# Kernel tuning notes

Hardware: AMD Instinct MI355X
Metric: run time of the kernel (lower is better)

The kernel has to match this reference:

```python
import jax, jax.numpy as jnp
import numpy as np

N_POL, N_TICK, N_COMM = 50000, 200000, 5000
N_STATES, N_SECTORS, N_INDUSTRIES = 50, 12, 150
EMB, HID, OUT = 32, 64, 32
N_NODES = N_POL + N_TICK + N_COMM
N_EDGES = 4_000_000


def setup_inputs() -> dict:
    key = jax.random.key(0)
    ks = jax.random.split(key, 24)
    s = lambda d: 1.0 / np.sqrt(d)
    inp = {
        "pol_features": jax.random.normal(ks[0], (N_POL, 7), jnp.float32),
        "state_ids": jax.random.randint(ks[1], (N_POL,), 0, N_STATES, jnp.int32),
        "sector_ids": jax.random.randint(ks[2], (N_TICK,), 0, N_SECTORS, jnp.int32),
        "industry_ids": jax.random.randint(ks[3], (N_TICK,), 0, N_INDUSTRIES, jnp.int32),
        "comp_extra": jax.random.normal(ks[4], (N_TICK, 1), jnp.float32),
        "edge_index": jax.random.randint(ks[5], (2, N_EDGES), 0, N_NODES, jnp.int32),
        "edge_weight": jax.random.uniform(ks[6], (N_EDGES,), jnp.float32),
        # learned params
        "pol_W": jax.random.normal(ks[7], (7, EMB), jnp.float32) * s(7),
        "pol_b": jnp.zeros((EMB,), jnp.float32),
        "state_emb": jax.random.normal(ks[8], (N_STATES, EMB), jnp.float32),
        "sector_emb": jax.random.normal(ks[9], (N_SECTORS, 8), jnp.float32),
        "industry_emb": jax.random.normal(ks[10], (N_INDUSTRIES, 8), jnp.float32),
        "comp_W": jax.random.normal(ks[11], (17, EMB), jnp.float32) * s(17),
        "comp_b": jnp.zeros((EMB,), jnp.float32),
        "comm_emb": jax.random.normal(ks[12], (N_COMM, EMB), jnp.float32),
        "ln_g": jnp.ones((EMB,), jnp.float32),
        "ln_b": jnp.zeros((EMB,), jnp.float32),
        "w1_rel": jax.random.normal(ks[13], (EMB, HID), jnp.float32) * s(EMB),
        "b1_rel": jnp.zeros((HID,), jnp.float32),
        "w1_root": jax.random.normal(ks[14], (EMB, HID), jnp.float32) * s(EMB),
        "w2_rel": jax.random.normal(ks[15], (HID, OUT), jnp.float32) * s(HID),
        "b2_rel": jnp.zeros((OUT,), jnp.float32),
        "w2_root": jax.random.normal(ks[16], (HID, OUT), jnp.float32) * s(HID),
    }
    return inp


def _layernorm(x, g, b, eps=1e-5):
    mu = jnp.mean(x, axis=-1, keepdims=True)
    var = jnp.mean(jnp.square(x - mu), axis=-1, keepdims=True)
    return (x - mu) * jax.lax.rsqrt(var + eps) * g + b


def _graph_conv(x, src, dst, ew, w_rel, b_rel, w_root):
    # PyG GraphConv: out = lin_rel(sum_{j->i} w_ji * x_j) + lin_root(x_i)
    msg = x[src] * ew[:, None]                                   # [E, d] gather
    agg = jax.ops.segment_sum(msg, dst, num_segments=x.shape[0])  # [N, d] scatter
    return agg @ w_rel + b_rel + x @ w_root


def reference(pol_features, state_ids, sector_ids, industry_ids, comp_extra,
              edge_index, edge_weight,
              pol_W, pol_b, state_emb, sector_emb, industry_emb, comp_W, comp_b,
              comm_emb, ln_g, ln_b, w1_rel, b1_rel, w1_root, w2_rel, b2_rel, w2_root):
    pol = jax.nn.relu(pol_features @ pol_W + pol_b) + state_emb[state_ids]
    comp_in = jnp.concatenate(
        [sector_emb[sector_ids], industry_emb[industry_ids], comp_extra], axis=1)  # [n_tick,17]
    comp = jax.nn.relu(comp_in @ comp_W + comp_b)
    x = jnp.concatenate([pol, comp, comm_emb], axis=0)  # [N, EMB]
    x = _layernorm(x, ln_g, ln_b)
    src, dst = edge_index[0], edge_index[1]
    x = jax.nn.relu(_graph_conv(x, src, dst, edge_weight, w1_rel, b1_rel, w1_root))
    # dropout omitted (eval mode)
    x = _graph_conv(x, src, dst, edge_weight, w2_rel, b2_rel, w2_root)
    return x
```

## Files before the change

kernel.cpp:

```cpp
#include <hip/hip_runtime.h>
#include <hip/hip_bf16.h>

#define N_POL  50000
#define N_TICK 200000
#define N_COMM 5000
#define N_NODES 255000
#define N_EDGES 4000000
#define EMB 32
#define HID 64
#define OUT_D 32

__global__ __launch_bounds__(256) void k_embed(
    const float* __restrict__ pol_features, const int* __restrict__ state_ids,
    const int* __restrict__ sector_ids, const int* __restrict__ industry_ids,
    const float* __restrict__ comp_extra,
    const float* __restrict__ pol_W, const float* __restrict__ pol_b,
    const float* __restrict__ state_emb, const float* __restrict__ sector_emb,
    const float* __restrict__ industry_emb, const float* __restrict__ comp_W,
    const float* __restrict__ comp_b, const float* __restrict__ comm_emb,
    const float* __restrict__ ln_g, const float* __restrict__ ln_b,
    float* __restrict__ x)
{
    int tid = blockIdx.x * 256 + threadIdx.x;
    int r = tid >> 5;
    int c = tid & 31;
    if (r >= N_NODES) return;

    float acc;
    if (r < N_POL) {
        acc = pol_b[c];
        #pragma unroll
        for (int k = 0; k < 7; ++k)
            acc = fmaf(pol_features[r*7 + k], pol_W[k*EMB + c], acc);
        acc = fmaxf(acc, 0.f);
        acc += state_emb[state_ids[r]*EMB + c];
    } else if (r < N_POL + N_TICK) {
        int i = r - N_POL;
        acc = comp_b[c];
        int sec = sector_ids[i], ind = industry_ids[i];
        #pragma unroll
        for (int k = 0; k < 8; ++k)
            acc = fmaf(sector_emb[sec*8 + k], comp_W[k*EMB + c], acc);
        #pragma unroll
        for (int k = 0; k < 8; ++k)
            acc = fmaf(industry_emb[ind*8 + k], comp_W[(8+k)*EMB + c], acc);
        acc = fmaf(comp_extra[i], comp_W[16*EMB + c], acc);
        acc = fmaxf(acc, 0.f);
    } else {
        acc = comm_emb[(r - N_POL - N_TICK)*EMB + c];
    }

    float s = acc;
    #pragma unroll
    for (int m = 16; m >= 1; m >>= 1) s += __shfl_xor(s, m, 32);
    float mu = s * (1.f/32.f);
    float d  = acc - mu;
    float v  = d * d;
    #pragma unroll
    for (int m = 16; m >= 1; m >>= 1) v += __shfl_xor(v, m, 32);
    v *= (1.f/32.f);
    x[r*EMB + c] = d * rsqrtf(v + 1e-5f) * ln_g[c] + ln_b[c];
}

__global__ __launch_bounds__(256) void k_hist(const int* __restrict__ ei,
                                              int* __restrict__ deg)
{
    int e = blockIdx.x * 256 + threadIdx.x;
    if (e >= N_EDGES) return;
    atomicAdd(&deg[ei[N_EDGES + e]], 1);
}

__global__ __launch_bounds__(256) void k_scan1(const int* __restrict__ deg,
                                               int* __restrict__ rowptr,
                                               int* __restrict__ bsum)
{
    __shared__ int s[256];
    int t = threadIdx.x;
    int base = blockIdx.x * 1024 + t * 4;
    int d0 = (base+0 < N_NODES) ? deg[base+0] : 0;
    int d1 = (base+1 < N_NODES) ? deg[base+1] : 0;
    int d2 = (base+2 < N_NODES) ? deg[base+2] : 0;
    int d3 = (base+3 < N_NODES) ? deg[base+3] : 0;
    int tsum = d0 + d1 + d2 + d3;
    s[t] = tsum;
    __syncthreads();
    for (int off = 1; off < 256; off <<= 1) {
        int v = (t >= off) ? s[t-off] : 0;
        __syncthreads();
        s[t] += v;
        __syncthreads();
    }
    int excl = s[t] - tsum;
    if (base+0 < N_NODES) rowptr[base+0] = excl;
    if (base+1 < N_NODES) rowptr[base+1] = excl + d0;
    if (base+2 < N_NODES) rowptr[base+2] = excl + d0 + d1;
    if (base+3 < N_NODES) rowptr[base+3] = excl + d0 + d1 + d2;
    if (t == 255) bsum[blockIdx.x] = s[255];
}

#define NBLK_SCAN 250

__global__ __launch_bounds__(256) void k_scan2(int* bsum)
{
    __shared__ int s[256];
    int t = threadIdx.x;
    int v = (t < NBLK_SCAN) ? bsum[t] : 0;
    s[t] = v;
    __syncthreads();
    for (int off = 1; off < 256; off <<= 1) {
        int u = (t >= off) ? s[t-off] : 0;
        __syncthreads();
        s[t] += u;
        __syncthreads();
    }
    if (t < NBLK_SCAN) bsum[t] = s[t] - v;
}

__global__ __launch_bounds__(256) void k_scan3(int* __restrict__ rowptr,
                                               const int* __restrict__ bsum)
{
    int i = blockIdx.x * 256 + threadIdx.x;
    if (i < N_NODES) rowptr[i] += bsum[i >> 10];
    if (i == 0) rowptr[N_NODES] = N_EDGES;
}

__global__ __launch_bounds__(256) void k_fill(const int* __restrict__ ei,
                                              const float* __restrict__ ew,
                                              const int* __restrict__ rowptr,
                                              int* __restrict__ cur,
                                              int2* __restrict__ ce)
{
    int e = blockIdx.x * 256 + threadIdx.x;
    if (e >= N_EDGES) return;
    int dst = ei[N_EDGES + e];
    int pos = rowptr[dst] + atomicAdd(&cur[dst], 1);
    ce[pos] = make_int2(ei[e], __float_as_int(ew[e]));
}

__global__ __launch_bounds__(256) void k_agg(const int* __restrict__ rowptr,
                                             const int2* __restrict__ ce,
                                             const float* __restrict__ feat,
                                             float* __restrict__ agg)
{
    int tid = blockIdx.x * 256 + threadIdx.x;
    int r = tid >> 5;
    int c = tid & 31;
    if (r >= N_NODES) return;
    int beg = rowptr[r], end = rowptr[r+1];
    float a0 = 0.f, a1 = 0.f, a2 = 0.f, a3 = 0.f;
    int i = beg;
    for (; i + 4 <= end; i += 4) {
        int2 e0 = ce[i], e1 = ce[i+1], e2 = ce[i+2], e3 = ce[i+3];
        a0 = fmaf(feat[(size_t)e0.x*EMB + c], __int_as_float(e0.y), a0);
        a1 = fmaf(feat[(size_t)e1.x*EMB + c], __int_as_float(e1.y), a1);
        a2 = fmaf(feat[(size_t)e2.x*EMB + c], __int_as_float(e2.y), a2);
        a3 = fmaf(feat[(size_t)e3.x*EMB + c], __int_as_float(e3.y), a3);
    }
    for (; i < end; ++i) {
        int2 e = ce[i];
        a0 = fmaf(feat[(size_t)e.x*EMB + c], __int_as_float(e.y), a0);
    }
    agg[(size_t)r*EMB + c] = (a0 + a1) + (a2 + a3);
}

__global__ __launch_bounds__(256) void k_conv1(
    const float* __restrict__ x, const float* __restrict__ agg,
    const float* __restrict__ w1_rel, const float* __restrict__ b1_rel,
    const float* __restrict__ w1_root,
    float* __restrict__ x1)
{
    int lane = threadIdx.x & 63;
    int wid  = threadIdx.x >> 6;

    float wr[32], wt[32];
    #pragma unroll
    for (int k = 0; k < 32; ++k) {
        wr[k] = w1_rel[k*HID + lane];
        wt[k] = w1_root[k*HID + lane];
    }
    float bias = b1_rel[lane];

    int nw = gridDim.x * 4;
    for (int r0 = blockIdx.x*4 + wid; r0 < N_NODES; r0 += nw) {
        int r = __builtin_amdgcn_readfirstlane(r0);
        const float4* xr = (const float4*)(x   + (size_t)r*EMB);
        const float4* ar = (const float4*)(agg + (size_t)r*EMB);
        float a0 = bias, a1 = 0.f, a2 = 0.f, a3 = 0.f;
        #pragma unroll
        for (int i = 0; i < 8; ++i) {
            float4 xv = xr[i];
            float4 av = ar[i];
            a0 = fmaf(xv.x, wt[4*i+0], a0);  a0 = fmaf(av.x, wr[4*i+0], a0);
            a1 = fmaf(xv.y, wt[4*i+1], a1);  a1 = fmaf(av.y, wr[4*i+1], a1);
            a2 = fmaf(xv.z, wt[4*i+2], a2);  a2 = fmaf(av.z, wr[4*i+2], a2);
            a3 = fmaf(xv.w, wt[4*i+3], a3);  a3 = fmaf(av.w, wr[4*i+3], a3);
        }
        x1[(size_t)r*HID + lane] = fmaxf((a0 + a1) + (a2 + a3), 0.f);
    }
}

__global__ __launch_bounds__(256) void k_z(
    const float* __restrict__ x1, const float* __restrict__ w2_rel,
    float* __restrict__ z)
{
    int lane = threadIdx.x & 63;
    int wid  = threadIdx.x >> 6;
    int c    = lane & 31;
    int half = lane >> 5;

    float w[32];
    #pragma unroll
    for (int j = 0; j < 32; ++j) w[j] = w2_rel[(half*32 + j)*OUT_D + c];

    int nw = gridDim.x * 4;
    for (int r0 = blockIdx.x*4 + wid; r0 < N_NODES; r0 += nw) {
        int r = __builtin_amdgcn_readfirstlane(r0);
        const float4* xr = (const float4*)(x1 + (size_t)r*HID + half*32);
        float p0 = 0.f, p1 = 0.f, p2 = 0.f, p3 = 0.f;
        #pragma unroll
        for (int i = 0; i < 8; ++i) {
            float4 v = xr[i];
            p0 = fmaf(v.x, w[4*i+0], p0);
            p1 = fmaf(v.y, w[4*i+1], p1);
            p2 = fmaf(v.z, w[4*i+2], p2);
            p3 = fmaf(v.w, w[4*i+3], p3);
        }
        float part = (p0 + p1) + (p2 + p3);
        part += __shfl_xor(part, 32, 64);
        if (lane < 32) z[(size_t)r*EMB + c] = part;
    }
}

__global__ __launch_bounds__(256) void k_out(
    const float* __restrict__ x1, const float* __restrict__ agg,
    const float* __restrict__ w2_root, const float* __restrict__ b2_rel,
    float* __restrict__ out)
{
    int lane = threadIdx.x & 63;
    int wid  = threadIdx.x >> 6;
    int c    = lane & 31;
    int half = lane >> 5;

    float w[32];
    #pragma unroll
    for (int j = 0; j < 32; ++j) w[j] = w2_root[(half*32 + j)*OUT_D + c];
    float bias = b2_rel[c];

    int nw = gridDim.x * 4;
    for (int r0 = blockIdx.x*4 + wid; r0 < N_NODES; r0 += nw) {
        int r = __builtin_amdgcn_readfirstlane(r0);
        const float4* xr = (const float4*)(x1 + (size_t)r*HID + half*32);
        float p0 = 0.f, p1 = 0.f, p2 = 0.f, p3 = 0.f;
        #pragma unroll
        for (int i = 0; i < 8; ++i) {
            float4 v = xr[i];
            p0 = fmaf(v.x, w[4*i+0], p0);
            p1 = fmaf(v.y, w[4*i+1], p1);
            p2 = fmaf(v.z, w[4*i+2], p2);
            p3 = fmaf(v.w, w[4*i+3], p3);
        }
        float part = (p0 + p1) + (p2 + p3);
        part += __shfl_xor(part, 32, 64);
        if (lane < 32)
            out[(size_t)r*OUT_D + c] = part + agg[(size_t)r*EMB + c] + bias;
    }
}

extern "C" void kernel_launch(void* const* d_in, const int* in_sizes, int n_in,
                              void* d_out, int out_size, void* d_ws, size_t ws_size,
                              hipStream_t stream) {
    const float* pol_features = (const float*)d_in[0];
    const int*   state_ids    = (const int*)  d_in[1];
    const int*   sector_ids   = (const int*)  d_in[2];
    const int*   industry_ids = (const int*)  d_in[3];
    const float* comp_extra   = (const float*)d_in[4];
    const int*   edge_index   = (const int*)  d_in[5];
    const float* edge_weight  = (const float*)d_in[6];
    const float* pol_W        = (const float*)d_in[7];
    const float* pol_b        = (const float*)d_in[8];
    const float* state_emb    = (const float*)d_in[9];
    const float* sector_emb   = (const float*)d_in[10];
    const float* industry_emb = (const float*)d_in[11];
    const float* comp_W       = (const float*)d_in[12];
    const float* comp_b       = (const float*)d_in[13];
    const float* comm_emb     = (const float*)d_in[14];
    const float* ln_g         = (const float*)d_in[15];
    const float* ln_b         = (const float*)d_in[16];
    const float* w1_rel       = (const float*)d_in[17];
    const float* b1_rel       = (const float*)d_in[18];
    const float* w1_root      = (const float*)d_in[19];
    const float* w2_rel       = (const float*)d_in[20];
    const float* b2_rel       = (const float*)d_in[21];
    const float* w2_root      = (const float*)d_in[22];

    float* x   = (float*)d_ws;
    float* x1  = x  + (size_t)N_NODES * EMB;
    float* agg = x1 + (size_t)N_NODES * HID;
    int2*  ce  = (int2*)(agg + (size_t)N_NODES * EMB);
    int*   rowptr = (int*)(ce + N_EDGES);
    int*   cur    = rowptr + N_NODES + 8;
    int*   bsum   = cur + N_NODES + 8;
    float* out = (float*)d_out;

    k_embed<<<(N_NODES*32 + 255)/256, 256, 0, stream>>>(
        pol_features, state_ids, sector_ids, industry_ids, comp_extra,
        pol_W, pol_b, state_emb, sector_emb, industry_emb, comp_W, comp_b,
        comm_emb, ln_g, ln_b, x);

    hipMemsetAsync(cur, 0, (size_t)N_NODES * sizeof(int), stream);
    k_hist<<<(N_EDGES + 255)/256, 256, 0, stream>>>(edge_index, cur);
    k_scan1<<<NBLK_SCAN, 256, 0, stream>>>(cur, rowptr, bsum);
    k_scan2<<<1, 256, 0, stream>>>(bsum);
    k_scan3<<<(N_NODES + 255)/256, 256, 0, stream>>>(rowptr, bsum);
    hipMemsetAsync(cur, 0, (size_t)N_NODES * sizeof(int), stream);
    k_fill<<<(N_EDGES + 255)/256, 256, 0, stream>>>(edge_index, edge_weight,
                                                    rowptr, cur, ce);

    k_agg<<<(N_NODES*32 + 255)/256, 256, 0, stream>>>(rowptr, ce, x, agg);
    k_conv1<<<4096, 256, 0, stream>>>(x, agg, w1_rel, b1_rel, w1_root, x1);
    k_z<<<4096, 256, 0, stream>>>(x1, w2_rel,  x);

    k_agg<<<(N_NODES*32 + 255)/256, 256, 0, stream>>>(rowptr, ce,  x, agg);
    k_out<<<4096, 256, 0, stream>>>(x1, agg, w2_root, b2_rel, out);
}
```

Measured before the change: 921.7 us.

## Replace per-node CSR build with two-pass bucketed radix sort and LDS-atomic aggregation

Drops the per-node histogram, three-kernel scan and atomic fill that built a CSR. In their place, a two-level radix partition sorts edges by destination into 128-node groups: coarse 1024-node buckets first, then 8 sub-buckets each, with staging in LDS so global writes stay coalesced. Aggregation then runs one workgroup per group and accumulates into shared memory with workgroup-scope float atomics. This cuts global atomics and scattered writes, but adds LDS atomic contention, a non-deterministic summation order and packed src/row encodings that depend on the node count bounds.

```diff
diff --git a/kernel.cpp b/kernel.cpp
--- a/kernel.cpp
+++ b/kernel.cpp
@@ -9,6 +9,12 @@
 #define EMB 32
 #define HID 64
 #define OUT_D 32
+
+#define NG 1993
+#define NB 250
+#define CHUNK 4096
+#define NWG_A 977
+#define PARTS 5
 
 __global__ __launch_bounds__(256) void k_embed(
     const float* __restrict__ pol_features, const int* __restrict__ state_ids,
@@ -62,50 +68,38 @@
     x[r*EMB + c] = d * rsqrtf(v + 1e-5f) * ln_g[c] + ln_b[c];
 }
 
-__global__ __launch_bounds__(256) void k_hist(const int* __restrict__ ei,
-                                              int* __restrict__ deg)
-{
-    int e = blockIdx.x * 256 + threadIdx.x;
-    if (e >= N_EDGES) return;
-    atomicAdd(&deg[ei[N_EDGES + e]], 1);
-}
-
-__global__ __launch_bounds__(256) void k_scan1(const int* __restrict__ deg,
-                                               int* __restrict__ rowptr,
-                                               int* __restrict__ bsum)
+__global__ __launch_bounds__(256) void k_bhist(const int* __restrict__ ei,
+                                               int* __restrict__ gcnt)
+{
+    __shared__ int h[NG];
+    for (int j = threadIdx.x; j < NG; j += 256) h[j] = 0;
+    __syncthreads();
+    int e0 = blockIdx.x * CHUNK;
+    int n  = min(CHUNK, N_EDGES - e0);
+    for (int j = threadIdx.x; j < n; j += 256) {
+        int d = ei[N_EDGES + e0 + j];
+        atomicAdd(&h[d >> 7], 1);
+    }
+    __syncthreads();
+    for (int j = threadIdx.x; j < NG; j += 256)
+        if (h[j]) atomicAdd(&gcnt[j], h[j]);
+}
+
+__global__ __launch_bounds__(256) void k_bscan(int* __restrict__ cnt_then_cur,
+                                               int* __restrict__ groupBase,
+                                               int* __restrict__ curA)
 {
     __shared__ int s[256];
     int t = threadIdx.x;
-    int base = blockIdx.x * 1024 + t * 4;
-    int d0 = (base+0 < N_NODES) ? deg[base+0] : 0;
-    int d1 = (base+1 < N_NODES) ? deg[base+1] : 0;
-    int d2 = (base+2 < N_NODES) ? deg[base+2] : 0;
-    int d3 = (base+3 < N_NODES) ? deg[base+3] : 0;
-    int tsum = d0 + d1 + d2 + d3;
+    int v[8];
+    int tsum = 0;
+    #pragma unroll
+    for (int k = 0; k < 8; ++k) {
+        int j = t*8 + k;
+        v[k] = (j < NG) ? cnt_then_cur[j] : 0;
+        tsum += v[k];
+    }
     s[t] = tsum;
-    __syncthreads();
-    for (int off = 1; off < 256; off <<= 1) {
-        int v = (t >= off) ? s[t-off] : 0;
-        __syncthreads();
-        s[t] += v;
-        __syncthreads();
-    }
-    int excl = s[t] - tsum;
-    if (base+0 < N_NODES) rowptr[base+0] = excl;
-    if (base+1 < N_NODES) rowptr[base+1] = excl + d0;
-    if (base+2 < N_NODES) rowptr[base+2] = excl + d0 + d1;
-    if (base+3 < N_NODES) rowptr[base+3] = excl + d0 + d1 + d2;
-    if (t == 255) bsum[blockIdx.x] = s[255];
-}
-
-#define NBLK_SCAN 250
-
-__global__ __launch_bounds__(256) void k_scan2(int* bsum)
-{
-    __shared__ int s[256];
-    int t = threadIdx.x;
-    int v = (t < NBLK_SCAN) ? bsum[t] : 0;
-    s[t] = v;
     __syncthreads();
     for (int off = 1; off < 256; off <<= 1) {
         int u = (t >= off) ? s[t-off] : 0;
@@ -113,54 +107,156 @@
         s[t] += u;
         __syncthreads();
     }
-    if (t < NBLK_SCAN) bsum[t] = s[t] - v;
-}
-
-__global__ __launch_bounds__(256) void k_scan3(int* __restrict__ rowptr,
-                                               const int* __restrict__ bsum)
-{
-    int i = blockIdx.x * 256 + threadIdx.x;
-    if (i < N_NODES) rowptr[i] += bsum[i >> 10];
-    if (i == 0) rowptr[N_NODES] = N_EDGES;
-}
-
-__global__ __launch_bounds__(256) void k_fill(const int* __restrict__ ei,
-                                              const float* __restrict__ ew,
-                                              const int* __restrict__ rowptr,
-                                              int* __restrict__ cur,
-                                              int2* __restrict__ ce)
-{
-    int e = blockIdx.x * 256 + threadIdx.x;
-    if (e >= N_EDGES) return;
-    int dst = ei[N_EDGES + e];
-    int pos = rowptr[dst] + atomicAdd(&cur[dst], 1);
-    ce[pos] = make_int2(ei[e], __float_as_int(ew[e]));
-}
-
-__global__ __launch_bounds__(256) void k_agg(const int* __restrict__ rowptr,
-                                             const int2* __restrict__ ce,
-                                             const float* __restrict__ feat,
-                                             float* __restrict__ agg)
-{
-    int tid = blockIdx.x * 256 + threadIdx.x;
-    int r = tid >> 5;
-    int c = tid & 31;
-    if (r >= N_NODES) return;
-    int beg = rowptr[r], end = rowptr[r+1];
-    float a0 = 0.f, a1 = 0.f, a2 = 0.f, a3 = 0.f;
-    int i = beg;
-    for (; i + 4 <= end; i += 4) {
-        int2 e0 = ce[i], e1 = ce[i+1], e2 = ce[i+2], e3 = ce[i+3];
-        a0 = fmaf(feat[(size_t)e0.x*EMB + c], __int_as_float(e0.y), a0);
-        a1 = fmaf(feat[(size_t)e1.x*EMB + c], __int_as_float(e1.y), a1);
-        a2 = fmaf(feat[(size_t)e2.x*EMB + c], __int_as_float(e2.y), a2);
-        a3 = fmaf(feat[(size_t)e3.x*EMB + c], __int_as_float(e3.y), a3);
-    }
-    for (; i < end; ++i) {
-        int2 e = ce[i];
-        a0 = fmaf(feat[(size_t)e.x*EMB + c], __int_as_float(e.y), a0);
-    }
-    agg[(size_t)r*EMB + c] = (a0 + a1) + (a2 + a3);
+    int excl = s[t] - tsum;
+    int running = excl;
+    #pragma unroll
+    for (int k = 0; k < 8; ++k) {
+        int j = t*8 + k;
+        if (j < NG) {
+            groupBase[j] = running;
+            cnt_then_cur[j] = running;
+        }
+        running += v[k];
+    }
+    if (t < NB) curA[t] = excl;
+    if (t == 250) groupBase[NG] = excl;
+}
+
+__global__ __launch_bounds__(256) void k_passA(const int* __restrict__ ei,
+                                               const float* __restrict__ ew,
+                                               int* __restrict__ curA,
+                                               int2* __restrict__ ce1)
+{
+    __shared__ int2 stg[CHUNK];
+    __shared__ unsigned char aux[CHUNK];
+    __shared__ int cnt[256], start[256], mycur[256], goff[256], sc[256];
+
+    int t = threadIdx.x;
+    int e0 = blockIdx.x * CHUNK;
+    int n  = min(CHUNK, N_EDGES - e0);
+
+    cnt[t] = 0;
+    __syncthreads();
+    for (int j = t; j < n; j += 256) {
+        int d = ei[N_EDGES + e0 + j];
+        atomicAdd(&cnt[d >> 10], 1);
+    }
+    __syncthreads();
+    int v = cnt[t];
+    sc[t] = v;
+    __syncthreads();
+    for (int off = 1; off < 256; off <<= 1) {
+        int u = (t >= off) ? sc[t-off] : 0;
+        __syncthreads();
+        sc[t] += u;
+        __syncthreads();
+    }
+    start[t] = sc[t] - v;
+    mycur[t] = sc[t] - v;
+    if (t < NB && v > 0) goff[t] = atomicAdd(&curA[t], v);
+    __syncthreads();
+
+    for (int j = t; j < n; j += 256) {
+        int d = ei[N_EDGES + e0 + j];
+        int srcv = ei[e0 + j];
+        float w = ew[e0 + j];
+        int b = d >> 10;
+        int slot = atomicAdd(&mycur[b], 1);
+        stg[slot] = make_int2(((d & 1023) << 18) | srcv, __float_as_int(w));
+        aux[slot] = (unsigned char)b;
+    }
+    __syncthreads();
+    for (int j = t; j < n; j += 256) {
+        int b = aux[j];
+        ce1[goff[b] + (j - start[b])] = stg[j];
+    }
+}
+
+__global__ __launch_bounds__(256) void k_passA2(const int2* __restrict__ ce1,
+                                                const int* __restrict__ groupBase,
+                                                int* __restrict__ curA2,
+                                                int2* __restrict__ ce2)
+{
+    __shared__ int2 stg[CHUNK];
+    __shared__ unsigned char aux[CHUNK];
+    __shared__ int cnt[8], start[8], mycur[8], goff[8];
+
+    int t = threadIdx.x;
+    int b = blockIdx.x / PARTS;
+    int k = blockIdx.x % PARTS;
+    int g0 = b * 8;
+    int g1 = min(g0 + 8, NG);
+    int lo = groupBase[g0];
+    int hi = groupBase[g1];
+    int len = hi - lo;
+    int chunk = (len + PARTS - 1) / PARTS;
+    int s0 = lo + k * chunk;
+    int s1 = min(s0 + chunk, hi);
+    int n = s1 - s0;
+    if (n <= 0) return;
+
+    if (t < 8) cnt[t] = 0;
+    __syncthreads();
+    for (int j = t; j < n; j += 256) {
+        int p = ce1[s0 + j].x;
+        atomicAdd(&cnt[(p >> 25) & 7], 1);
+    }
+    __syncthreads();
+    if (t == 0) {
+        int running = 0;
+        #pragma unroll
+        for (int s = 0; s < 8; ++s) { start[s] = running; mycur[s] = running; running += cnt[s]; }
+    }
+    __syncthreads();
+    if (t < 8 && cnt[t] > 0) goff[t] = atomicAdd(&curA2[g0 + t], cnt[t]);
+    __syncthreads();
+
+    for (int j = t; j < n; j += 256) {
+        int2 e = ce1[s0 + j];
+        int sub = (e.x >> 25) & 7;
+        int slot = atomicAdd(&mycur[sub], 1);
+        stg[slot] = e;
+        aux[slot] = (unsigned char)sub;
+    }
+    __syncthreads();
+    for (int j = t; j < n; j += 256) {
+        int sub = aux[j];
+        ce2[goff[sub] + (j - start[sub])] = stg[j];
+    }
+}
+
+__global__ __launch_bounds__(256) void k_bagg(const int* __restrict__ groupBase,
+                                              const int2* __restrict__ ce2,
+                                              const float* __restrict__ feat,
+                                              float* __restrict__ agg)
+{
+    __shared__ float acc[128 * EMB];
+    int t = threadIdx.x;
+    int g = blockIdx.x;
+
+    float4* a4 = (float4*)acc;
+    #pragma unroll
+    for (int k = 0; k < 4; ++k) a4[t + k*256] = make_float4(0.f, 0.f, 0.f, 0.f);
+    __syncthreads();
+
+    int lo = groupBase[g], hi = groupBase[g + 1];
+    int grp = t >> 5;
+    int c   = t & 31;
+    for (int i = lo + grp; i < hi; i += 8) {
+        int2 e = ce2[i];
+        int row  = (e.x >> 18) & 127;
+        int srcv = e.x & 0x3FFFF;
+        float w  = __int_as_float(e.y);
+        float val = feat[(size_t)srcv * EMB + c] * w;
+        __hip_atomic_fetch_add(&acc[row * EMB + c], val,
+                               __ATOMIC_RELAXED, __HIP_MEMORY_SCOPE_WORKGROUP);
+    }
+    __syncthreads();
+
+    int r0 = g * 128;
+    int nr = min(128, N_NODES - r0);
+    for (int j = t; j < nr * EMB; j += 256)
+        agg[(size_t)r0 * EMB + j] = acc[j];
 }
 
 __global__ __launch_bounds__(256) void k_conv1(
@@ -296,30 +392,29 @@
     float* x   = (float*)d_ws;
     float* x1  = x  + (size_t)N_NODES * EMB;
     float* agg = x1 + (size_t)N_NODES * HID;
-    int2*  ce  = (int2*)(agg + (size_t)N_NODES * EMB);
-    int*   rowptr = (int*)(ce + N_EDGES);
-    int*   cur    = rowptr + N_NODES + 8;
-    int*   bsum   = cur + N_NODES + 8;
+    int2*  ce2 = (int2*)(agg + (size_t)N_NODES * EMB);
+    int*   groupBase = (int*)(ce2 + N_EDGES);
+    int*   curA2     = groupBase + NG + 8;
+    int*   curA      = curA2 + NG + 8;
+    int2*  ce1 = (int2*)x1;
     float* out = (float*)d_out;
+
+    hipMemsetAsync(curA2, 0, NG * sizeof(int), stream);
 
     k_embed<<<(N_NODES*32 + 255)/256, 256, 0, stream>>>(
         pol_features, state_ids, sector_ids, industry_ids, comp_extra,
         pol_W, pol_b, state_emb, sector_emb, industry_emb, comp_W, comp_b,
         comm_emb, ln_g, ln_b, x);
 
-    hipMemsetAsync(cur, 0, (size_t)N_NODES * sizeof(int), stream);
-    k_hist<<<(N_EDGES + 255)/256, 256, 0, stream>>>(edge_index, cur);
-    k_scan1<<<NBLK_SCAN, 256, 0, stream>>>(cur, rowptr, bsum);
-    k_scan2<<<1, 256, 0, stream>>>(bsum);
-    k_scan3<<<(N_NODES + 255)/256, 256, 0, stream>>>(rowptr, bsum);
-    hipMemsetAsync(cur, 0, (size_t)N_NODES * sizeof(int), stream);
-    k_fill<<<(N_EDGES + 255)/256, 256, 0, stream>>>(edge_index, edge_weight,
-                                                    rowptr, cur, ce);
-
-    k_agg<<<(N_NODES*32 + 255)/256, 256, 0, stream>>>(rowptr, ce, x, agg);
+    k_bhist<<<NWG_A, 256, 0, stream>>>(edge_index, curA2);
+    k_bscan<<<1, 256, 0, stream>>>(curA2, groupBase, curA);
+    k_passA<<<NWG_A, 256, 0, stream>>>(edge_index, edge_weight, curA, ce1);
+    k_passA2<<<NB*PARTS, 256, 0, stream>>>(ce1, groupBase, curA2, ce2);
+
+    k_bagg<<<NG, 256, 0, stream>>>(groupBase, ce2, x, agg);
     k_conv1<<<4096, 256, 0, stream>>>(x, agg, w1_rel, b1_rel, w1_root, x1);
     k_z<<<4096, 256, 0, stream>>>(x1, w2_rel,  x);
 
-    k_agg<<<(N_NODES*32 + 255)/256, 256, 0, stream>>>(rowptr, ce,  x, agg);
+    k_bagg<<<NG, 256, 0, stream>>>(groupBase, ce2,  x, agg);
     k_out<<<4096, 256, 0, stream>>>(x1, agg, w2_root, b2_rel, out);
 }
```

Result: slower. 1.805 ms (+95.8%).
